# Kernel tuning notes

Measured on AMD Instinct MI355X. Metric: run time of the kernel, lower is better.

## Reference

```python
import jax, jax.numpy as jnp
import numpy as np

N_NODES = 100000
N_EDGES = 3200000
PERIODS = 12
C_IN, C_OUT, F_OUT = 1, 4, 12


def setup_inputs() -> dict:
    key = jax.random.key(0)
    ks = jax.random.split(key, 20)
    s = 0.1
    return {
        "x": jax.random.normal(ks[0], (N_NODES, C_IN, PERIODS), dtype=jnp.float32),
        "edge_index": jax.random.randint(ks[1], (2, N_EDGES), 0, N_NODES, dtype=jnp.int32),
        "conv_z_w": s * jax.random.normal(ks[2], (C_IN, C_OUT), dtype=jnp.float32),
        "conv_z_b": s * jax.random.normal(ks[3], (C_OUT,), dtype=jnp.float32),
        "lin_z_w": s * jax.random.normal(ks[4], (2 * C_OUT, C_OUT), dtype=jnp.float32),
        "lin_z_b": s * jax.random.normal(ks[5], (C_OUT,), dtype=jnp.float32),
        "conv_r_w": s * jax.random.normal(ks[6], (C_IN, C_OUT), dtype=jnp.float32),
        "conv_r_b": s * jax.random.normal(ks[7], (C_OUT,), dtype=jnp.float32),
        "lin_r_w": s * jax.random.normal(ks[8], (2 * C_OUT, C_OUT), dtype=jnp.float32),
        "lin_r_b": s * jax.random.normal(ks[9], (C_OUT,), dtype=jnp.float32),
        "conv_h_w": s * jax.random.normal(ks[10], (C_IN, C_OUT), dtype=jnp.float32),
        "conv_h_b": s * jax.random.normal(ks[11], (C_OUT,), dtype=jnp.float32),
        "lin_h_w": s * jax.random.normal(ks[12], (2 * C_OUT, C_OUT), dtype=jnp.float32),
        "lin_h_b": s * jax.random.normal(ks[13], (C_OUT,), dtype=jnp.float32),
        "att": jax.random.normal(ks[14], (PERIODS,), dtype=jnp.float32),
        "out_w": s * jax.random.normal(ks[15], (C_OUT, F_OUT), dtype=jnp.float32),
        "out_b": s * jax.random.normal(ks[16], (F_OUT,), dtype=jnp.float32),
        "f": 12,
    }


def reference(x, edge_index, conv_z_w, conv_z_b, lin_z_w, lin_z_b,
              conv_r_w, conv_r_b, lin_r_w, lin_r_b,
              conv_h_w, conv_h_b, lin_h_w, lin_h_b,
              att, out_w, out_b, f):
    N, _, P = x.shape
    loops = jnp.arange(N, dtype=edge_index.dtype)
    src = jnp.concatenate([edge_index[0], loops])  # self loops, fill=1
    dst = jnp.concatenate([edge_index[1], loops])
    deg = jax.ops.segment_sum(jnp.ones_like(src, dtype=x.dtype), dst, num_segments=N)
    dinv = jnp.where(deg > 0, jax.lax.rsqrt(deg), 0.0)
    norm = dinv[src] * dinv[dst]  # [E+N] symmetric GCN normalization

    def gcn(xt, W, b):
        xw = xt @ W  # [N, C_OUT]
        msg = xw[src] * norm[:, None]
        return jax.ops.segment_sum(msg, dst, num_segments=N) + b

    H0 = jnp.zeros((N, conv_z_w.shape[1]), dtype=x.dtype)

    def tgcn_step(xt):  # xt: [N, C_IN]; A3TGCN does not carry H across periods
        z = jax.nn.sigmoid(jnp.concatenate([gcn(xt, conv_z_w, conv_z_b), H0], 1) @ lin_z_w + lin_z_b)
        r = jax.nn.sigmoid(jnp.concatenate([gcn(xt, conv_r_w, conv_r_b), H0], 1) @ lin_r_w + lin_r_b)
        h_t = jnp.tanh(jnp.concatenate([gcn(xt, conv_h_w, conv_h_b), r * H0], 1) @ lin_h_w + lin_h_b)
        return z * H0 + (1.0 - z) * h_t

    xs = jnp.transpose(x, (2, 0, 1))  # [P, N, C_IN]
    Hs = jax.vmap(tgcn_step)(xs)  # [P, N, C_OUT]
    probs = jax.nn.softmax(att)
    H_accum = jnp.einsum('p,pnd->nd', probs, Hs)  # attention over periods
    out = H_accum @ out_w + out_b  # [N, 12]
    return out[:, :f]
```

## Files before the change

kernel.cpp:

```cpp
#include <hip/hip_runtime.h>
#include <hip/hip_fp16.h>
#include <math.h>


#define PERIODS 12
#define BSZ     256
#define BSH     8
#define STRIDE  9216
#define SRCBITS 17
#define SMASK   ((1 << SRCBITS) - 1)
#define CH      4096

struct Consts {
    float az[4], cz[4], ah[4], ch[4], probs[PERIODS];
};

typedef float vf2 __attribute__((ext_vector_type(2)));

__device__ __forceinline__ float dec1_manual(unsigned b) {
    unsigned e = (b >> 3) & 15u, m = b & 7u;
    float v = e ? __uint_as_float(((e + 120u) << 23) | (m << 20))
                : (float)m * 0.001953125f;
    return (b & 0x80u) ? -v : v;
}

__device__ __forceinline__ void dec4(unsigned u, float* o) {
#if __has_builtin(__builtin_amdgcn_cvt_pk_f32_fp8)
    vf2 lo = __builtin_amdgcn_cvt_pk_f32_fp8((int)u, false);
    vf2 hi = __builtin_amdgcn_cvt_pk_f32_fp8((int)u, true);
    o[0] = lo.x; o[1] = lo.y; o[2] = hi.x; o[3] = hi.y;
#else
    o[0] = dec1_manual(u & 255u);
    o[1] = dec1_manual((u >> 8) & 255u);
    o[2] = dec1_manual((u >> 16) & 255u);
    o[3] = dec1_manual(u >> 24);
#endif
}

__device__ __forceinline__ unsigned enc1_manual(float x) {
    unsigned s = (__float_as_uint(x) >> 24) & 0x80u;
    float a = fabsf(x);
    if (!(a > 0.f)) return s;
    a = fminf(a, 448.f);
    int eb = (int)(__float_as_uint(a) >> 23) - 127;
    int e = eb < -6 ? -6 : eb;
    float q = rintf(a * exp2f((float)(3 - e)));
    if (q >= 16.f) { e++; q = rintf(a * exp2f((float)(3 - e))); }
    if (e > 8) return s | 0x7Eu;
    int m = (int)q;
    unsigned ee, mm;
    if (m >= 8) { ee = (unsigned)(e + 7); mm = (unsigned)(m - 8); }
    else        { ee = 0u; mm = (unsigned)m; }
    return s | (ee << 3) | mm;
}

__device__ __forceinline__ unsigned pk4(float a, float b, float c, float d) {
#if __has_builtin(__builtin_amdgcn_cvt_pk_fp8_f32)
    int v = __builtin_amdgcn_cvt_pk_fp8_f32(a, b, 0, false);
    v = __builtin_amdgcn_cvt_pk_fp8_f32(c, d, v, true);
    return (unsigned)v;
#else
    return enc1_manual(a) | (enc1_manual(b) << 8) |
           (enc1_manual(c) << 16) | (enc1_manual(d) << 24);
#endif
}


__global__ __launch_bounds__(512) void k_setup(const float* conv_z_w, const float* conv_z_b,
                        const float* lin_z_w, const float* lin_z_b,
                        const float* conv_h_w, const float* conv_h_b,
                        const float* lin_h_w, const float* lin_h_b,
                        const float* att, Consts* C, int* gcur, int NB)
{
    int t = threadIdx.x;
    for (int i = t; i < NB; i += 512) gcur[i] = 0;
    if (t == 0) {
        for (int c = 0; c < 4; ++c) {
            float az = 0.f, cz = 0.f, ah = 0.f, ch = 0.f;
            for (int k = 0; k < 4; ++k) {
                az += conv_z_w[k] * lin_z_w[k * 4 + c];
                cz += conv_z_b[k] * lin_z_w[k * 4 + c];
                ah += conv_h_w[k] * lin_h_w[k * 4 + c];
                ch += conv_h_b[k] * lin_h_w[k * 4 + c];
            }
            C->az[c] = az; C->cz[c] = cz + lin_z_b[c];
            C->ah[c] = ah; C->ch[c] = ch + lin_h_b[c];
        }
        float m = att[0];
        for (int p = 1; p < PERIODS; ++p) m = fmaxf(m, att[p]);
        float e[PERIODS]; float s = 0.f;
        for (int p = 0; p < PERIODS; ++p) { e[p] = expf(att[p] - m); s += e[p]; }
        for (int p = 0; p < PERIODS; ++p) C->probs[p] = e[p] / s;
    }
}

__global__ __launch_bounds__(512) void k_binA(const int* __restrict__ ei,
                                              int* __restrict__ gcur,
                                              int* __restrict__ binned, int E) {
    __shared__ int hist[512];
    __shared__ int scn[512];
    __shared__ int gdel[512];
    __shared__ int sv[CH];
    __shared__ int sa[CH];
    int t = threadIdx.x;
    hist[t] = 0;
    __syncthreads();
    int base = blockIdx.x * CH;
    int lim = min(E - base, CH);
    #pragma unroll
    for (int k = 0; k < CH / 512; ++k) {
        int i = t + k * 512;
        if (i < lim) atomicAdd(&hist[ei[E + base + i] >> BSH], 1);
    }
    __syncthreads();
    int v = hist[t];
    scn[t] = v;
    __syncthreads();
    for (int off = 1; off < 512; off <<= 1) {
        int tmp = (t >= off) ? scn[t - off] : 0;
        __syncthreads();
        scn[t] += tmp;
        __syncthreads();
    }
    int excl = scn[t] - v;
    int g = (v > 0) ? atomicAdd(&gcur[t], v) : 0;
    gdel[t] = t * STRIDE + g - excl;
    hist[t] = excl;
    __syncthreads();
    #pragma unroll
    for (int k = 0; k < CH / 512; ++k) {
        int i = t + k * 512;
        if (i < lim) {
            int s = ei[base + i];
            int d = ei[E + base + i];
            int b = d >> BSH;
            int pos = atomicAdd(&hist[b], 1);
            sv[pos] = ((d & (BSZ - 1)) << SRCBITS) | s;
            sa[pos] = gdel[b] + pos;
        }
    }
    __syncthreads();
    for (int j = t; j < lim; j += 512)
        binned[sa[j]] = sv[j];
}

__global__ __launch_bounds__(512) void k_binB(const int* __restrict__ binned,
                                              const int* __restrict__ gcur,
                                              int* __restrict__ nodesorted,
                                              int* __restrict__ nofs) {
    __shared__ int hist[BSZ];
    __shared__ int scn[512];
    __shared__ int cur[BSZ];
    __shared__ int sorted[STRIDE];
    int b = blockIdx.x, t = threadIdx.x;
    if (t < BSZ) hist[t] = 0;
    __syncthreads();
    int cnt = gcur[b];
    const int* bb = binned + b * STRIDE;
    for (int i = t; i < cnt; i += 512)
        atomicAdd(&hist[bb[i] >> SRCBITS], 1);
    __syncthreads();
    int v = (t < BSZ) ? hist[t] : 0;
    scn[t] = v;
    __syncthreads();
    for (int off = 1; off < 512; off <<= 1) {
        int tmp = (t >= off) ? scn[t - off] : 0;
        __syncthreads();
        scn[t] += tmp;
        __syncthreads();
    }
    if (t < BSZ) {
        int excl = scn[t] - v;
        cur[t] = excl;
        nofs[b * BSZ + t] = excl;
    }
    __syncthreads();
    for (int i = t; i < cnt; i += 512) {
        int pv = bb[i];
        int pos = atomicAdd(&cur[pv >> SRCBITS], 1);
        sorted[pos] = pv & SMASK;
    }
    __syncthreads();
    int* dst = nodesorted + b * STRIDE;
    for (int j = t; j < cnt; j += 512)
        dst[j] = sorted[j];
}

__global__ void k_prep(const int* __restrict__ nofs, const int* __restrict__ gcur,
                       const float* __restrict__ x, float* __restrict__ dinv,
                       uint4* __restrict__ xs8, int N) {
    int n = blockIdx.x * blockDim.x + threadIdx.x;
    if (n >= N) return;
    int b = n >> BSH, ln = n & (BSZ - 1);
    int start = nofs[b * BSZ + ln];
    int end = (ln == BSZ - 1) ? gcur[b] : nofs[b * BSZ + ln + 1];
    float di = rsqrtf((float)(end - start) + 1.0f);
    dinv[n] = di;
    const float4* xv = (const float4*)(x + (size_t)n * PERIODS);
    float4 v0 = xv[0], v1 = xv[1], v2 = xv[2];
    uint4 r;
    r.x = pk4(v0.x * di, v0.y * di, v0.z * di, v0.w * di);
    r.y = pk4(v1.x * di, v1.y * di, v1.z * di, v1.w * di);
    r.z = pk4(v2.x * di, v2.y * di, v2.z * di, v2.w * di);
    r.w = 0;
    xs8[n] = r;
}

__device__ __forceinline__ void accdec(float* acc, uint4 r) {
    float f[PERIODS];
    dec4(r.x, f + 0); dec4(r.y, f + 4); dec4(r.z, f + 8);
    #pragma unroll
    for (int k = 0; k < PERIODS; ++k) acc[k] += f[k];
}

__global__ __launch_bounds__(512) void k_aggF(const int* __restrict__ nodesorted,
                                              const int* __restrict__ nofs,
                                              const int* __restrict__ gcur,
                                              const float* __restrict__ dinv,
                                              const uint4* __restrict__ xs8,
                                              const Consts* __restrict__ C,
                                              const float* __restrict__ out_w,
                                              const float* __restrict__ out_b,
                                              float* __restrict__ out, int N) {
    int t = threadIdx.x;
    int b = blockIdx.x >> 1;
    int half = blockIdx.x & 1;
    int ln = half * 128 + (t >> 2);
    int lane = t & 3;
    int n = (b << BSH) + ln;

    int start = nofs[b * BSZ + ln];
    int end = (ln == BSZ - 1) ? gcur[b] : nofs[b * BSZ + ln + 1];
    const int* ns = nodesorted + b * STRIDE;

    float acc[PERIODS];
    #pragma unroll
    for (int k = 0; k < PERIODS; ++k) acc[k] = 0.f;

    int i = start + lane;
    for (; i + 12 < end; i += 16) {
        int s0 = ns[i];
        int s1 = ns[i + 4];
        int s2 = ns[i + 8];
        int s3 = ns[i + 12];
        uint4 r0 = xs8[s0];
        uint4 r1 = xs8[s1];
        uint4 r2 = xs8[s2];
        uint4 r3 = xs8[s3];
        accdec(acc, r0);
        accdec(acc, r1);
        accdec(acc, r2);
        accdec(acc, r3);
    }
    for (; i < end; i += 4) {
        uint4 r0 = xs8[ns[i]];
        accdec(acc, r0);
    }

    #pragma unroll
    for (int k = 0; k < PERIODS; ++k) {
        acc[k] += __shfl_xor(acc[k], 1);
        acc[k] += __shfl_xor(acc[k], 2);
    }

    if (lane != 0 || n >= N) return;

    {
        float f[PERIODS];
        uint4 r = xs8[n];
        dec4(r.x, f + 0); dec4(r.y, f + 4); dec4(r.z, f + 8);
        #pragma unroll
        for (int k = 0; k < PERIODS; ++k) acc[k] += f[k];
    }

    float di = dinv[n];
    float hacc[4] = {0.f, 0.f, 0.f, 0.f};
    #pragma unroll
    for (int p = 0; p < PERIODS; ++p) {
        float ap = di * acc[p];
        float pr = C->probs[p];
        #pragma unroll
        for (int c = 0; c < 4; ++c) {
            float zz = 1.f / (1.f + __expf(-(ap * C->az[c] + C->cz[c])));
            float hh = tanhf(ap * C->ah[c] + C->ch[c]);
            hacc[c] += pr * (1.f - zz) * hh;
        }
    }
    float o[PERIODS];
    #pragma unroll
    for (int f = 0; f < PERIODS; ++f) {
        float v = out_b[f];
        #pragma unroll
        for (int c = 0; c < 4; ++c) v += hacc[c] * out_w[c * PERIODS + f];
        o[f] = v;
    }
    float4* ov = (float4*)(out + (size_t)n * PERIODS);
    ov[0] = make_float4(o[0], o[1], o[2],  o[3]);
    ov[1] = make_float4(o[4], o[5], o[6],  o[7]);
    ov[2] = make_float4(o[8], o[9], o[10], o[11]);
}

extern "C" void kernel_launch(void* const* d_in, const int* in_sizes, int n_in,
                              void* d_out, int out_size, void* d_ws, size_t ws_size,
                              hipStream_t stream) {
    const float* x        = (const float*)d_in[0];
    const int*   ei       = (const int*)d_in[1];
    const float* conv_z_w = (const float*)d_in[2];
    const float* conv_z_b = (const float*)d_in[3];
    const float* lin_z_w  = (const float*)d_in[4];
    const float* lin_z_b  = (const float*)d_in[5];
    const float* conv_h_w = (const float*)d_in[10];
    const float* conv_h_b = (const float*)d_in[11];
    const float* lin_h_w  = (const float*)d_in[12];
    const float* lin_h_b  = (const float*)d_in[13];
    const float* att      = (const float*)d_in[14];
    const float* out_w    = (const float*)d_in[15];
    const float* out_b    = (const float*)d_in[16];
    float* out = (float*)d_out;

    const int N  = in_sizes[0] / PERIODS;
    const int E  = in_sizes[1] / 2;
    const int NB = (N + BSZ - 1) / BSZ;
    const int gA = (E + CH - 1) / CH;

    char* ws = (char*)d_ws;
    size_t off = 0;
    Consts* consts     = (Consts*)(ws + off);  off += (sizeof(Consts) + 255) & ~255ull;
    int*    gcur       = (int*)(ws + off);     off += ((size_t)NB * 4 + 255) & ~255ull;
    float*  dinv       = (float*)(ws + off);   off += ((size_t)N * 4 + 255) & ~255ull;
    uint4*  xs8        = (uint4*)(ws + off);   off += ((size_t)(N + 256) * 16 + 255) & ~255ull;
    int*    binned     = (int*)(ws + off);     off += ((size_t)NB * STRIDE * 4 + 255) & ~255ull;
    int*    nodesorted = (int*)(ws + off);     off += ((size_t)NB * STRIDE * 4 + 255) & ~255ull;
    int*    nofs       = (int*)(ws + off);     off += ((size_t)NB * BSZ * 4 + 255) & ~255ull;
    (void)ws_size; (void)n_in; (void)out_size;

    k_setup<<<1, 512, 0, stream>>>(conv_z_w, conv_z_b, lin_z_w, lin_z_b,
                                   conv_h_w, conv_h_b, lin_h_w, lin_h_b, att,
                                   consts, gcur, NB);
    k_binA<<<gA, 512, 0, stream>>>(ei, gcur, binned, E);
    k_binB<<<NB, 512, 0, stream>>>(binned, gcur, nodesorted, nofs);
    k_prep<<<(N + 255) / 256, 256, 0, stream>>>(nofs, gcur, x, dinv, xs8, N);
    k_aggF<<<NB * 2, 512, 0, stream>>>(nodesorted, nofs, gcur, dinv, xs8, consts,
                                       out_w, out_b, out, N);
}
```

Measured before the change: 184.5 us.

## Drop per-node sort pass; aggregate binned edges via shared-memory atomics

Removes the second binning kernel that sorted edges by destination within each 256-node bucket. The aggregation kernel now reads the coarse-binned edge list directly and scatters decoded fp8 features into a padded shared-memory accumulator with atomicAdd. Node degrees are instead counted with global atomics during the first binning pass, which also keeps the edge indices in registers so they are not reloaded. This saves a full read/write pass over the edge list and one launch, at the cost of many LDS float atomics and global atomic contention on deg.

```diff
diff --git a/kernel.cpp b/kernel.cpp
--- a/kernel.cpp
+++ b/kernel.cpp
@@ -10,6 +10,7 @@
 #define SRCBITS 17
 #define SMASK   ((1 << SRCBITS) - 1)
 #define CH      4096
+#define ACCS    13
 
 struct Consts {
     float az[4], cz[4], ah[4], ch[4], probs[PERIODS];
@@ -70,32 +71,39 @@
                         const float* lin_z_w, const float* lin_z_b,
                         const float* conv_h_w, const float* conv_h_b,
                         const float* lin_h_w, const float* lin_h_b,
-                        const float* att, Consts* C, int* gcur, int NB)
+                        const float* att, Consts* C, int* gcur, int* deg,
+                        int NB, int N)
 {
-    int t = threadIdx.x;
-    for (int i = t; i < NB; i += 512) gcur[i] = 0;
-    if (t == 0) {
-        for (int c = 0; c < 4; ++c) {
-            float az = 0.f, cz = 0.f, ah = 0.f, ch = 0.f;
-            for (int k = 0; k < 4; ++k) {
-                az += conv_z_w[k] * lin_z_w[k * 4 + c];
-                cz += conv_z_b[k] * lin_z_w[k * 4 + c];
-                ah += conv_h_w[k] * lin_h_w[k * 4 + c];
-                ch += conv_h_b[k] * lin_h_w[k * 4 + c];
+    int g = blockIdx.x * 512 + threadIdx.x;
+    int gs = gridDim.x * 512;
+    for (int i = g; i < N; i += gs) deg[i] = 0;
+    if (blockIdx.x == 0) {
+        int t = threadIdx.x;
+        for (int i = t; i < NB; i += 512) gcur[i] = 0;
+        if (t == 0) {
+            for (int c = 0; c < 4; ++c) {
+                float az = 0.f, cz = 0.f, ah = 0.f, ch = 0.f;
+                for (int k = 0; k < 4; ++k) {
+                    az += conv_z_w[k] * lin_z_w[k * 4 + c];
+                    cz += conv_z_b[k] * lin_z_w[k * 4 + c];
+                    ah += conv_h_w[k] * lin_h_w[k * 4 + c];
+                    ch += conv_h_b[k] * lin_h_w[k * 4 + c];
+                }
+                C->az[c] = az; C->cz[c] = cz + lin_z_b[c];
+                C->ah[c] = ah; C->ch[c] = ch + lin_h_b[c];
             }
-            C->az[c] = az; C->cz[c] = cz + lin_z_b[c];
-            C->ah[c] = ah; C->ch[c] = ch + lin_h_b[c];
+            float m = att[0];
+            for (int p = 1; p < PERIODS; ++p) m = fmaxf(m, att[p]);
+            float e[PERIODS]; float s = 0.f;
+            for (int p = 0; p < PERIODS; ++p) { e[p] = expf(att[p] - m); s += e[p]; }
+            for (int p = 0; p < PERIODS; ++p) C->probs[p] = e[p] / s;
         }
-        float m = att[0];
-        for (int p = 1; p < PERIODS; ++p) m = fmaxf(m, att[p]);
-        float e[PERIODS]; float s = 0.f;
-        for (int p = 0; p < PERIODS; ++p) { e[p] = expf(att[p] - m); s += e[p]; }
-        for (int p = 0; p < PERIODS; ++p) C->probs[p] = e[p] / s;
     }
 }
 
 __global__ __launch_bounds__(512) void k_binA(const int* __restrict__ ei,
                                               int* __restrict__ gcur,
+                                              int* __restrict__ deg,
                                               int* __restrict__ binned, int E) {
     __shared__ int hist[512];
     __shared__ int scn[512];
@@ -107,10 +115,16 @@
     __syncthreads();
     int base = blockIdx.x * CH;
     int lim = min(E - base, CH);
+    int rs[CH / 512], rd[CH / 512];
     #pragma unroll
     for (int k = 0; k < CH / 512; ++k) {
         int i = t + k * 512;
-        if (i < lim) atomicAdd(&hist[ei[E + base + i] >> BSH], 1);
+        if (i < lim) {
+            rs[k] = ei[base + i];
+            rd[k] = ei[E + base + i];
+            atomicAdd(&hist[rd[k] >> BSH], 1);
+            atomicAdd(&deg[rd[k]], 1);
+        }
     }
     __syncthreads();
     int v = hist[t];
@@ -131,8 +145,8 @@
     for (int k = 0; k < CH / 512; ++k) {
         int i = t + k * 512;
         if (i < lim) {
-            int s = ei[base + i];
-            int d = ei[E + base + i];
+            int s = rs[k];
+            int d = rd[k];
             int b = d >> BSH;
             int pos = atomicAdd(&hist[b], 1);
             sv[pos] = ((d & (BSZ - 1)) << SRCBITS) | s;
@@ -144,57 +158,12 @@
         binned[sa[j]] = sv[j];
 }
 
-__global__ __launch_bounds__(512) void k_binB(const int* __restrict__ binned,
-                                              const int* __restrict__ gcur,
-                                              int* __restrict__ nodesorted,
-                                              int* __restrict__ nofs) {
-    __shared__ int hist[BSZ];
-    __shared__ int scn[512];
-    __shared__ int cur[BSZ];
-    __shared__ int sorted[STRIDE];
-    int b = blockIdx.x, t = threadIdx.x;
-    if (t < BSZ) hist[t] = 0;
-    __syncthreads();
-    int cnt = gcur[b];
-    const int* bb = binned + b * STRIDE;
-    for (int i = t; i < cnt; i += 512)
-        atomicAdd(&hist[bb[i] >> SRCBITS], 1);
-    __syncthreads();
-    int v = (t < BSZ) ? hist[t] : 0;
-    scn[t] = v;
-    __syncthreads();
-    for (int off = 1; off < 512; off <<= 1) {
-        int tmp = (t >= off) ? scn[t - off] : 0;
-        __syncthreads();
-        scn[t] += tmp;
-        __syncthreads();
-    }
-    if (t < BSZ) {
-        int excl = scn[t] - v;
-        cur[t] = excl;
-        nofs[b * BSZ + t] = excl;
-    }
-    __syncthreads();
-    for (int i = t; i < cnt; i += 512) {
-        int pv = bb[i];
-        int pos = atomicAdd(&cur[pv >> SRCBITS], 1);
-        sorted[pos] = pv & SMASK;
-    }
-    __syncthreads();
-    int* dst = nodesorted + b * STRIDE;
-    for (int j = t; j < cnt; j += 512)
-        dst[j] = sorted[j];
-}
-
-__global__ void k_prep(const int* __restrict__ nofs, const int* __restrict__ gcur,
+__global__ void k_prep(const int* __restrict__ deg,
                        const float* __restrict__ x, float* __restrict__ dinv,
                        uint4* __restrict__ xs8, int N) {
     int n = blockIdx.x * blockDim.x + threadIdx.x;
     if (n >= N) return;
-    int b = n >> BSH, ln = n & (BSZ - 1);
-    int start = nofs[b * BSZ + ln];
-    int end = (ln == BSZ - 1) ? gcur[b] : nofs[b * BSZ + ln + 1];
-    float di = rsqrtf((float)(end - start) + 1.0f);
+    float di = rsqrtf((float)deg[n] + 1.0f);
     dinv[n] = di;
     const float4* xv = (const float4*)(x + (size_t)n * PERIODS);
     float4 v0 = xv[0], v1 = xv[1], v2 = xv[2];
@@ -206,78 +175,68 @@
     xs8[n] = r;
 }
 
-__device__ __forceinline__ void accdec(float* acc, uint4 r) {
+__device__ __forceinline__ void scat(float* acc, int d, uint4 r) {
     float f[PERIODS];
     dec4(r.x, f + 0); dec4(r.y, f + 4); dec4(r.z, f + 8);
-    #pragma unroll
-    for (int k = 0; k < PERIODS; ++k) acc[k] += f[k];
-}
-
-__global__ __launch_bounds__(512) void k_aggF(const int* __restrict__ nodesorted,
-                                              const int* __restrict__ nofs,
-                                              const int* __restrict__ gcur,
-                                              const float* __restrict__ dinv,
-                                              const uint4* __restrict__ xs8,
-                                              const Consts* __restrict__ C,
-                                              const float* __restrict__ out_w,
-                                              const float* __restrict__ out_b,
-                                              float* __restrict__ out, int N) {
-    int t = threadIdx.x;
-    int b = blockIdx.x >> 1;
-    int half = blockIdx.x & 1;
-    int ln = half * 128 + (t >> 2);
-    int lane = t & 3;
-    int n = (b << BSH) + ln;
-
-    int start = nofs[b * BSZ + ln];
-    int end = (ln == BSZ - 1) ? gcur[b] : nofs[b * BSZ + ln + 1];
-    const int* ns = nodesorted + b * STRIDE;
-
-    float acc[PERIODS];
-    #pragma unroll
-    for (int k = 0; k < PERIODS; ++k) acc[k] = 0.f;
-
-    int i = start + lane;
-    for (; i + 12 < end; i += 16) {
-        int s0 = ns[i];
-        int s1 = ns[i + 4];
-        int s2 = ns[i + 8];
-        int s3 = ns[i + 12];
-        uint4 r0 = xs8[s0];
-        uint4 r1 = xs8[s1];
-        uint4 r2 = xs8[s2];
-        uint4 r3 = xs8[s3];
-        accdec(acc, r0);
-        accdec(acc, r1);
-        accdec(acc, r2);
-        accdec(acc, r3);
-    }
-    for (; i < end; i += 4) {
-        uint4 r0 = xs8[ns[i]];
-        accdec(acc, r0);
-    }
-
-    #pragma unroll
-    for (int k = 0; k < PERIODS; ++k) {
-        acc[k] += __shfl_xor(acc[k], 1);
-        acc[k] += __shfl_xor(acc[k], 2);
-    }
-
-    if (lane != 0 || n >= N) return;
-
+    int base = d * ACCS;
+    #pragma unroll
+    for (int k = 0; k < PERIODS; ++k) atomicAdd(&acc[base + k], f[k]);
+}
+
+__global__ __launch_bounds__(512) void k_agg(const int* __restrict__ binned,
+                                             const int* __restrict__ gcur,
+                                             const float* __restrict__ dinv,
+                                             const uint4* __restrict__ xs8,
+                                             const Consts* __restrict__ C,
+                                             const float* __restrict__ out_w,
+                                             const float* __restrict__ out_b,
+                                             float* __restrict__ out, int N) {
+    __shared__ float acc[BSZ * ACCS];
+    int b = blockIdx.x, t = threadIdx.x;
+    for (int i = t; i < BSZ * ACCS; i += 512) acc[i] = 0.f;
+    __syncthreads();
+    int cnt = gcur[b];
+    const int* bb = binned + b * STRIDE;
+    int i = t;
+    for (; i + 1536 < cnt; i += 2048) {
+        int p0 = bb[i];
+        int p1 = bb[i + 512];
+        int p2 = bb[i + 1024];
+        int p3 = bb[i + 1536];
+        uint4 r0 = xs8[p0 & SMASK];
+        uint4 r1 = xs8[p1 & SMASK];
+        uint4 r2 = xs8[p2 & SMASK];
+        uint4 r3 = xs8[p3 & SMASK];
+        scat(acc, p0 >> SRCBITS, r0);
+        scat(acc, p1 >> SRCBITS, r1);
+        scat(acc, p2 >> SRCBITS, r2);
+        scat(acc, p3 >> SRCBITS, r3);
+    }
+    for (; i < cnt; i += 512) {
+        int pv = bb[i];
+        uint4 r = xs8[pv & SMASK];
+        scat(acc, pv >> SRCBITS, r);
+    }
+    __syncthreads();
+
+    if (t >= BSZ) return;
+    int n = (b << BSH) + t;
+    if (n >= N) return;
+
+    float a[PERIODS];
     {
         float f[PERIODS];
         uint4 r = xs8[n];
         dec4(r.x, f + 0); dec4(r.y, f + 4); dec4(r.z, f + 8);
         #pragma unroll
-        for (int k = 0; k < PERIODS; ++k) acc[k] += f[k];
+        for (int k = 0; k < PERIODS; ++k) a[k] = acc[t * ACCS + k] + f[k];
     }
 
     float di = dinv[n];
     float hacc[4] = {0.f, 0.f, 0.f, 0.f};
     #pragma unroll
     for (int p = 0; p < PERIODS; ++p) {
-        float ap = di * acc[p];
+        float ap = di * a[p];
         float pr = C->probs[p];
         #pragma unroll
         for (int c = 0; c < 4; ++c) {
@@ -325,21 +284,19 @@
 
     char* ws = (char*)d_ws;
     size_t off = 0;
-    Consts* consts     = (Consts*)(ws + off);  off += (sizeof(Consts) + 255) & ~255ull;
-    int*    gcur       = (int*)(ws + off);     off += ((size_t)NB * 4 + 255) & ~255ull;
-    float*  dinv       = (float*)(ws + off);   off += ((size_t)N * 4 + 255) & ~255ull;
-    uint4*  xs8        = (uint4*)(ws + off);   off += ((size_t)(N + 256) * 16 + 255) & ~255ull;
-    int*    binned     = (int*)(ws + off);     off += ((size_t)NB * STRIDE * 4 + 255) & ~255ull;
-    int*    nodesorted = (int*)(ws + off);     off += ((size_t)NB * STRIDE * 4 + 255) & ~255ull;
-    int*    nofs       = (int*)(ws + off);     off += ((size_t)NB * BSZ * 4 + 255) & ~255ull;
+    Consts* consts = (Consts*)(ws + off);  off += (sizeof(Consts) + 255) & ~255ull;
+    int*    gcur   = (int*)(ws + off);     off += ((size_t)NB * 4 + 255) & ~255ull;
+    int*    deg    = (int*)(ws + off);     off += ((size_t)N * 4 + 255) & ~255ull;
+    float*  dinv   = (float*)(ws + off);   off += ((size_t)N * 4 + 255) & ~255ull;
+    uint4*  xs8    = (uint4*)(ws + off);   off += ((size_t)(N + 256) * 16 + 255) & ~255ull;
+    int*    binned = (int*)(ws + off);     off += ((size_t)NB * STRIDE * 4 + 255) & ~255ull;
     (void)ws_size; (void)n_in; (void)out_size;
 
-    k_setup<<<1, 512, 0, stream>>>(conv_z_w, conv_z_b, lin_z_w, lin_z_b,
-                                   conv_h_w, conv_h_b, lin_h_w, lin_h_b, att,
-                                   consts, gcur, NB);
-    k_binA<<<gA, 512, 0, stream>>>(ei, gcur, binned, E);
-    k_binB<<<NB, 512, 0, stream>>>(binned, gcur, nodesorted, nofs);
-    k_prep<<<(N + 255) / 256, 256, 0, stream>>>(nofs, gcur, x, dinv, xs8, N);
-    k_aggF<<<NB * 2, 512, 0, stream>>>(nodesorted, nofs, gcur, dinv, xs8, consts,
-                                       out_w, out_b, out, N);
-}
+    k_setup<<<128, 512, 0, stream>>>(conv_z_w, conv_z_b, lin_z_w, lin_z_b,
+                                     conv_h_w, conv_h_b, lin_h_w, lin_h_b, att,
+                                     consts, gcur, deg, NB, N);
+    k_binA<<<gA, 512, 0, stream>>>(ei, gcur, deg, binned, E);
+    k_prep<<<(N + 255) / 256, 256, 0, stream>>>(deg, x, dinv, xs8, N);
+    k_agg<<<NB, 512, 0, stream>>>(binned, gcur, dinv, xs8, consts,
+                                  out_w, out_b, out, N);
+}
```

Result: slower. 509.7 us (+176.3%).
